# Performance work log

Measured on AMD Instinct MI355X. Metric: run time of the kernel, lower is better.

Reference implementation:

```python
import jax, jax.numpy as jnp
import numpy as np

N_NODES = 100000
N_EDGES = 1600000
HIDDEN = 128
N_REL = 8


def setup_inputs() -> dict:
    key = jax.random.key(0)
    ks = jax.random.split(key, 12)
    s = 1.0 / np.sqrt(HIDDEN)
    inp = {
        "node_idx": jnp.arange(N_NODES, dtype=jnp.int32),
        "edge_index": jax.random.randint(ks[0], (2, N_EDGES), 0, N_NODES, dtype=jnp.int32),
        "edge_type": jax.random.randint(ks[1], (N_EDGES,), 0, N_REL, dtype=jnp.int32),
        "embedding": jax.random.normal(ks[2], (N_NODES, HIDDEN), jnp.float32),
        "W_rel_0": jax.random.normal(ks[3], (N_REL, HIDDEN, HIDDEN), jnp.float32) * s,
        "W_root_0": jax.random.normal(ks[4], (HIDDEN, HIDDEN), jnp.float32) * s,
        "b_0": jnp.zeros((HIDDEN,), jnp.float32),
        "W_rel_1": jax.random.normal(ks[5], (N_REL, HIDDEN, HIDDEN), jnp.float32) * s,
        "W_root_1": jax.random.normal(ks[6], (HIDDEN, HIDDEN), jnp.float32) * s,
        "b_1": jnp.zeros((HIDDEN,), jnp.float32),
    }
    return inp


def _rgcn_conv(x, src, dst, et, W_rel, W_root, b):
    # PyG RGCNConv: out_i = x_i @ W_root + b + sum_r mean_{j in N_r(i)} x_j @ W_r
    n = x.shape[0]
    r = W_rel.shape[0]
    # Transform all nodes by all relations once (R small), then gather per edge.
    x_all = jnp.einsum('nd,rdf->rnf', x, W_rel)          # [R, N, d]
    msg = x_all[et, src]                                  # [E, d]
    # per-(relation, dst) mean normalization
    seg = et * n + dst                                    # [E]
    deg = jax.ops.segment_sum(jnp.ones(et.shape, jnp.float32), seg, num_segments=r * n)
    norm = 1.0 / jnp.maximum(deg[seg], 1.0)               # [E]
    agg = jax.ops.segment_sum(msg * norm[:, None], dst, num_segments=n)  # [N, d]
    return agg + x @ W_root + b


def reference(node_idx, edge_index, edge_type, embedding,
              W_rel_0, W_root_0, b_0, W_rel_1, W_root_1, b_1):
    src, dst = edge_index[0], edge_index[1]
    x = embedding[node_idx]
    x = jax.nn.relu(_rgcn_conv(x, src, dst, edge_type, W_rel_0, W_root_0, b_0))
    x = jax.nn.relu(_rgcn_conv(x, src, dst, edge_type, W_rel_1, W_root_1, b_1))
    return x
```

## Files before the change

kernel.cpp:

```cpp
#include <hip/hip_runtime.h>
#include <hip/hip_bf16.h>

typedef short bf16x8 __attribute__((ext_vector_type(8)));
typedef float f32x4 __attribute__((ext_vector_type(4)));

constexpr int NN = 100000;
constexpr int NE = 1600000;
constexpr int HH = 128;
constexpr int NR = 8;
constexpr int NBIN = 782;
constexpr int CAPB = 6144;

__device__ __forceinline__ unsigned short f2bf(float f) {
    unsigned b = __float_as_uint(f);
    b += 0x7fffu + ((b >> 16) & 1u);
    return (unsigned short)(b >> 16);
}

__global__ void convertWX(const float* __restrict__ Wr0, const float* __restrict__ Wq0,
                          const float* __restrict__ Wr1, const float* __restrict__ Wq1,
                          unsigned short* __restrict__ Wt,
                          const int* __restrict__ node_idx,
                          const float* __restrict__ emb,
                          unsigned* __restrict__ xb32) {
    if (blockIdx.x < 1152) {
        int o = blockIdx.x * 256 + threadIdx.x;
        int L = o / 147456;
        int rem = o - L * 147456;
        int s = rem >> 14;
        int p = rem & 16383;
        int f = p >> 7;
        int d = p & 127;
        const float* Wq = L ? Wq1 : Wq0;
        const float* Wr = L ? Wr1 : Wr0;
        float v = (s == 0) ? Wq[d * 128 + f] : Wr[((s - 1) * 128 + d) * 128 + f];
        Wt[o] = f2bf(v);
    } else {
        int i = (blockIdx.x - 1152) * 256 + threadIdx.x;
        if (i >= NN * 64) return;
        int n = i >> 6, dp = i & 63;
        int row = node_idx[n];
        float2 v = *((const float2*)(emb + (size_t)row * HH) + dp);
        xb32[(size_t)n * 64 + dp] = (unsigned)f2bf(v.x) | ((unsigned)f2bf(v.y) << 16);
    }
}

__global__ __launch_bounds__(256) void binCount(const int* __restrict__ edst,
                                                unsigned* __restrict__ binCounts) {
    __shared__ unsigned hist[NBIN];
    for (int i = threadIdx.x; i < NBIN; i += 256) hist[i] = 0;
    __syncthreads();
    int stride = gridDim.x * 256;
    for (int e = blockIdx.x * 256 + threadIdx.x; e < NE; e += stride)
        atomicAdd(&hist[((unsigned)edst[e]) >> 7], 1u);
    __syncthreads();
    for (int i = threadIdx.x; i < NBIN; i += 256)
        if (hist[i]) atomicAdd(&binCounts[i], hist[i]);
}

__global__ void binScan(const unsigned* __restrict__ binCounts,
                        unsigned* __restrict__ binStarts,
                        unsigned* __restrict__ binCursor) {
    __shared__ unsigned sh[1024];
    int tid = threadIdx.x;
    unsigned v = (tid < NBIN) ? binCounts[tid] : 0u;
    sh[tid] = v;
    __syncthreads();
    for (int ofs = 1; ofs < 1024; ofs <<= 1) {
        unsigned t = (tid >= ofs) ? sh[tid - ofs] : 0u;
        __syncthreads();
        sh[tid] += t;
        __syncthreads();
    }
    if (tid < NBIN) {
        unsigned s = sh[tid] - v;
        binStarts[tid] = s;
        binCursor[tid] = s;
    }
    if (tid == 0) binStarts[NBIN] = NE;
}

__global__ __launch_bounds__(256) void binScatter(
        const int* __restrict__ esrc, const int* __restrict__ edst,
        const int* __restrict__ etype, unsigned* __restrict__ binCursor,
        unsigned* __restrict__ binned) {
    __shared__ unsigned hist[NBIN];
    __shared__ unsigned cur[NBIN];
    for (int i = threadIdx.x; i < NBIN; i += 256) hist[i] = 0;
    __syncthreads();
    int per = (NE + gridDim.x - 1) / gridDim.x;
    int lo = blockIdx.x * per;
    int hi = lo + per; if (hi > NE) hi = NE;
    for (int e = lo + threadIdx.x; e < hi; e += 256)
        atomicAdd(&hist[((unsigned)edst[e]) >> 7], 1u);
    __syncthreads();
    for (int i = threadIdx.x; i < NBIN; i += 256) {
        unsigned c = hist[i];
        cur[i] = c ? atomicAdd(&binCursor[i], c) : 0u;
    }
    __syncthreads();
    for (int e = lo + threadIdx.x; e < hi; e += 256) {
        unsigned d = (unsigned)edst[e];
        unsigned b = d >> 7;
        unsigned pos = atomicAdd(&cur[b], 1u);
        binned[pos] = (unsigned)esrc[e] | (((unsigned)etype[e]) << 17) |
                      ((d & 127u) << 20);
    }
}

__global__ __launch_bounds__(256) void binSort(
        const unsigned* __restrict__ binStarts, const unsigned* __restrict__ binned,
        unsigned* __restrict__ epk, unsigned* __restrict__ starts) {
    __shared__ unsigned hist[1024];
    __shared__ unsigned scn[1024];
    __shared__ unsigned part[256];
    __shared__ unsigned buf[CAPB];
    __shared__ unsigned outb[CAPB];
    int bin = blockIdx.x;
    int tid = threadIdx.x;
    unsigned base = binStarts[bin];
    int cnt = (int)(binStarts[bin + 1] - base);

    for (int i = tid; i < 1024; i += 256) hist[i] = 0;
    __syncthreads();
    for (int i = tid; i < cnt; i += 256) {
        unsigned p = binned[base + i];
        if (i < CAPB) buf[i] = p;
        atomicAdd(&hist[(p >> 17) & 0x3ffu], 1u);
    }
    __syncthreads();
    unsigned h4[4], tsum = 0;
#pragma unroll
    for (int j = 0; j < 4; ++j) { h4[j] = hist[tid * 4 + j]; tsum += h4[j]; }
    part[tid] = tsum;
    __syncthreads();
    for (int ofs = 1; ofs < 256; ofs <<= 1) {
        unsigned t = (tid >= ofs) ? part[tid - ofs] : 0u;
        __syncthreads();
        part[tid] += t;
        __syncthreads();
    }
    unsigned run = part[tid] - tsum;
#pragma unroll
    for (int j = 0; j < 4; ++j) { scn[tid * 4 + j] = run; run += h4[j]; }
    __syncthreads();
    for (int i = tid; i < 1024; i += 256) {
        starts[(size_t)bin * 1024 + i] = base + scn[i];
        hist[i] = scn[i];
    }
    __syncthreads();
    if (cnt <= CAPB) {
        for (int i = tid; i < cnt; i += 256) {
            unsigned p = buf[i];
            unsigned pos = atomicAdd(&hist[(p >> 17) & 0x3ffu], 1u);
            outb[pos] = p & 0x1ffffu;
        }
        __syncthreads();
        for (int i = tid; i < cnt; i += 256) epk[base + i] = outb[i];
    } else {
        for (int i = tid; i < cnt; i += 256) {
            unsigned p = binned[base + i];
            unsigned pos = atomicAdd(&hist[(p >> 17) & 0x3ffu], 1u);
            epk[base + pos] = p & 0x1ffffu;
        }
    }
}

__global__ __launch_bounds__(256) void gatherNode(
        const unsigned* __restrict__ starts, const unsigned* __restrict__ epk,
        const unsigned* __restrict__ xb32, unsigned* __restrict__ h32) {
    int node = blockIdx.x * 4 + (threadIdx.x >> 6);
    if (node >= NN) return;
    int lane = threadIdx.x & 63;

    unsigned bv = 0;
    if (lane < 9) bv = starts[(size_t)node * 8 + lane];
    unsigned b[9];
#pragma unroll
    for (int r = 0; r < 9; ++r) b[r] = __shfl(bv, r);
    unsigned s0 = b[0], s1 = b[8];
    int cnt = (int)__builtin_amdgcn_readfirstlane((int)(s1 - s0));

    float a[8][2];
#pragma unroll
    for (int r = 0; r < 8; ++r) { a[r][0] = 0.f; a[r][1] = 0.f; }

    for (int c0 = 0; c0 < cnt; c0 += 64) {
        unsigned myE = s0 + (unsigned)c0 + (unsigned)lane;
        unsigned pk = (myE < s1) ? epk[myE] : 0u;
        unsigned rl = 0;
#pragma unroll
        for (int r = 1; r < 8; ++r) rl += (myE >= b[r]) ? 1u : 0u;
        pk |= rl << 24;
        int cend = cnt - c0;
        if (cend > 64) cend = 64;
        for (int base = 0; base < cend; base += 8) {
            int m = cend - base;
            if (m > 8) m = 8;
            unsigned pj[8], qj[8];
#pragma unroll
            for (int j = 0; j < 8; ++j)
                pj[j] = (j < m) ? (unsigned)__shfl((int)pk, base + j) : 0u;
#pragma unroll
            for (int j = 0; j < 8; ++j)
                if (j < m) qj[j] = xb32[(size_t)(pj[j] & 0x1ffffu) * 64 + lane];
#pragma unroll
            for (int j = 0; j < 8; ++j) {
                if (j < m) {
                    float lo = __uint_as_float(qj[j] << 16);
                    float hi = __uint_as_float(qj[j] & 0xffff0000u);
                    switch (__builtin_amdgcn_readfirstlane((int)(pj[j] >> 24))) {
                        case 0: a[0][0] += lo; a[0][1] += hi; break;
                        case 1: a[1][0] += lo; a[1][1] += hi; break;
                        case 2: a[2][0] += lo; a[2][1] += hi; break;
                        case 3: a[3][0] += lo; a[3][1] += hi; break;
                        case 4: a[4][0] += lo; a[4][1] += hi; break;
                        case 5: a[5][0] += lo; a[5][1] += hi; break;
                        case 6: a[6][0] += lo; a[6][1] += hi; break;
                        default: a[7][0] += lo; a[7][1] += hi; break;
                    }
                }
            }
        }
    }

#pragma unroll
    for (int r = 0; r < 8; ++r) {
        unsigned c = b[r + 1] - b[r];
        float inv = (c > 1u) ? (1.f / (float)c) : 1.f;
        unsigned out = (unsigned)f2bf(a[r][0] * inv) |
                       ((unsigned)f2bf(a[r][1] * inv) << 16);
        h32[((size_t)node * 8 + r) * 64 + lane] = out;
    }
}

__global__ __launch_bounds__(256) void rgcnGemm(const unsigned short* x,
                                                const unsigned short* __restrict__ h,
                                                const unsigned short* __restrict__ Wt,
                                                const float* __restrict__ bias,
                                                float* __restrict__ outF,
                                                unsigned short* outB) {
    constexpr int LDA = 136;
    __shared__ __align__(16) unsigned short A_lds[64 * LDA];
    __shared__ __align__(16) unsigned short B_lds[128 * LDA];

    int tid = threadIdx.x;
    int wid = tid >> 6, lane = tid & 63;
    int quad = lane >> 4, l16 = lane & 15;
    int wr = wid >> 1, wc = wid & 1;
    int m0 = blockIdx.x * 64;
    int chunk = tid & 15, rip = tid >> 4;

    f32x4 acc[2][4];
#pragma unroll
    for (int st = 0; st < 2; ++st)
#pragma unroll
        for (int nt = 0; nt < 4; ++nt) acc[st][nt] = (f32x4){0.f, 0.f, 0.f, 0.f};

    for (int s = 0; s < 9; ++s) {
        __syncthreads();
#pragma unroll
        for (int p = 0; p < 4; ++p) {
            int r = p * 16 + rip;
            int node = m0 + r;
            node = node < NN ? node : NN - 1;
            const unsigned short* rp = (s == 0)
                ? (x + (size_t)node * HH)
                : (h + ((size_t)node * 8 + (s - 1)) * HH);
            uint4 v = *((const uint4*)rp + chunk);
            *(uint4*)(&A_lds[r * LDA + chunk * 8]) = v;
        }
        const unsigned short* Bbase = Wt + s * 16384;
#pragma unroll
        for (int p = 0; p < 8; ++p) {
            int r = p * 16 + rip;
            uint4 v = *((const uint4*)(Bbase + r * 128) + chunk);
            *(uint4*)(&B_lds[r * LDA + chunk * 8]) = v;
        }
        __syncthreads();
#pragma unroll
        for (int kt = 0; kt < 4; ++kt) {
            int ko = kt * 32 + quad * 8;
            bf16x8 a[2], b[4];
            a[0] = *(const bf16x8*)(&A_lds[(wr * 32 + l16) * LDA + ko]);
            a[1] = *(const bf16x8*)(&A_lds[(wr * 32 + 16 + l16) * LDA + ko]);
#pragma unroll
            for (int nt = 0; nt < 4; ++nt)
                b[nt] = *(const bf16x8*)(&B_lds[(wc * 64 + nt * 16 + l16) * LDA + ko]);
#pragma unroll
            for (int st = 0; st < 2; ++st)
#pragma unroll
                for (int nt = 0; nt < 4; ++nt)
                    acc[st][nt] = __builtin_amdgcn_mfma_f32_16x16x32_bf16(
                        a[st], b[nt], acc[st][nt], 0, 0, 0);
        }
    }
#pragma unroll
    for (int st = 0; st < 2; ++st) {
        int rowbase = m0 + wr * 32 + st * 16 + quad * 4;
#pragma unroll
        for (int nt = 0; nt < 4; ++nt) {
            int n = wc * 64 + nt * 16 + l16;
            float bv = bias[n];
#pragma unroll
            for (int rg = 0; rg < 4; ++rg) {
                int node = rowbase + rg;
                if (node < NN) {
                    float v = acc[st][nt][rg] + bv;
                    v = v > 0.f ? v : 0.f;
                    if (outF) outF[(size_t)node * HH + n] = v;
                    else outB[(size_t)node * HH + n] = f2bf(v);
                }
            }
        }
    }
}

extern "C" void kernel_launch(void* const* d_in, const int* in_sizes, int n_in,
                              void* d_out, int out_size, void* d_ws, size_t ws_size,
                              hipStream_t stream) {
    const int* node_idx = (const int*)d_in[0];
    const int* eidx     = (const int*)d_in[1];
    const int* etype    = (const int*)d_in[2];
    const float* emb    = (const float*)d_in[3];
    const float* Wr0    = (const float*)d_in[4];
    const float* Wq0    = (const float*)d_in[5];
    const float* b0     = (const float*)d_in[6];
    const float* Wr1    = (const float*)d_in[7];
    const float* Wq1    = (const float*)d_in[8];
    const float* b1     = (const float*)d_in[9];
    const int* esrc = eidx;
    const int* edst = eidx + NE;

    char* ws = (char*)d_ws;
    size_t off = 0;
    auto alloc = [&](size_t bytes) -> void* {
        void* p = ws + off;
        off = (off + bytes + 255) & ~(size_t)255;
        return p;
    };
    unsigned* binCounts = (unsigned*)alloc((size_t)NBIN * 4);
    unsigned* binStarts = (unsigned*)alloc((size_t)(NBIN + 1) * 4);
    unsigned* binCursor = (unsigned*)alloc((size_t)NBIN * 4);
    unsigned* starts    = (unsigned*)alloc((size_t)NBIN * 1024 * 4);
    unsigned* epk       = (unsigned*)alloc((size_t)NE * 4);
    unsigned* xb32      = (unsigned*)alloc((size_t)NN * 64 * 4);
    unsigned* h32       = (unsigned*)alloc((size_t)NN * 8 * 64 * 4);
    unsigned short* Wt  = (unsigned short*)alloc((size_t)2 * 9 * 16384 * 2);
    unsigned* binned = h32;
    (void)ws_size; (void)n_in; (void)in_sizes; (void)out_size;

    hipMemsetAsync(binCounts, 0, (size_t)NBIN * 4, stream);
    convertWX<<<1152 + (NN * 64 + 255) / 256, 256, 0, stream>>>(
        Wr0, Wq0, Wr1, Wq1, Wt, node_idx, emb, xb32);
    binCount<<<256, 256, 0, stream>>>(edst, binCounts);
    binScan<<<1, 1024, 0, stream>>>(binCounts, binStarts, binCursor);
    binScatter<<<128, 256, 0, stream>>>(esrc, edst, etype, binCursor, binned);
    binSort<<<NBIN, 256, 0, stream>>>(binStarts, binned, epk, starts);

    int nblk = (NN + 63) / 64;
    gatherNode<<<(NN + 3) / 4, 256, 0, stream>>>(starts, epk, xb32, h32);
    rgcnGemm<<<nblk, 256, 0, stream>>>((const unsigned short*)xb32,
                                       (const unsigned short*)h32, Wt, b0,
                                       nullptr, (unsigned short*)xb32);
    gatherNode<<<(NN + 3) / 4, 256, 0, stream>>>(starts, epk, xb32, h32);
    rgcnGemm<<<nblk, 256, 0, stream>>>((const unsigned short*)xb32,
                                       (const unsigned short*)h32, Wt + 147456, b1,
                                       (float*)d_out, nullptr);
}
```

Before: 601.7 us.

## Transform nodes by all relations first, then gather normalized messages per edge

Each layer changes from aggregate-then-transform to transform-then-aggregate. The old order gathered x per relation into an [N,8,128] buffer and then ran a 9-step GEMM. Now one GEMM computes x·W_r for every relation plus the root term into a bf16 [N,8,128] table. A scatter kernel then gathers one pre-transformed row per edge, scales it by 1/degree, and adds root, bias and ReLU. binSort now packs (src,rel) and the clamped per-relation degree into each edge word, which removes the per-relation accumulator switch in the gather. The aim is to drop the h buffer's GEMM input and the branchy per-relation accumulation. The cost is that per-edge reads now hit a random-access table eight times larger than before, so cache locality gets worse.

Result: faster. 552.9 us (-8.1%).

```diff
diff --git a/kernel.cpp b/kernel.cpp
--- a/kernel.cpp
+++ b/kernel.cpp
@@ -113,6 +113,7 @@
         unsigned* __restrict__ epk, unsigned* __restrict__ starts) {
     __shared__ unsigned hist[1024];
     __shared__ unsigned scn[1024];
+    __shared__ unsigned cnts[1024];
     __shared__ unsigned part[256];
     __shared__ unsigned buf[CAPB];
     __shared__ unsigned outb[CAPB];
@@ -146,100 +147,35 @@
     __syncthreads();
     for (int i = tid; i < 1024; i += 256) {
         starts[(size_t)bin * 1024 + i] = base + scn[i];
+        cnts[i] = hist[i];
         hist[i] = scn[i];
     }
     __syncthreads();
     if (cnt <= CAPB) {
         for (int i = tid; i < cnt; i += 256) {
             unsigned p = buf[i];
-            unsigned pos = atomicAdd(&hist[(p >> 17) & 0x3ffu], 1u);
-            outb[pos] = p & 0x1ffffu;
+            unsigned key = (p >> 17) & 0x3ffu;
+            unsigned pos = atomicAdd(&hist[key], 1u);
+            unsigned deg = cnts[key]; if (deg > 4095u) deg = 4095u;
+            outb[pos] = ((p & 0x1ffffu) << 3) | (key & 7u) | (deg << 20);
         }
         __syncthreads();
         for (int i = tid; i < cnt; i += 256) epk[base + i] = outb[i];
     } else {
         for (int i = tid; i < cnt; i += 256) {
             unsigned p = binned[base + i];
-            unsigned pos = atomicAdd(&hist[(p >> 17) & 0x3ffu], 1u);
-            epk[base + pos] = p & 0x1ffffu;
-        }
-    }
-}
-
-__global__ __launch_bounds__(256) void gatherNode(
-        const unsigned* __restrict__ starts, const unsigned* __restrict__ epk,
-        const unsigned* __restrict__ xb32, unsigned* __restrict__ h32) {
-    int node = blockIdx.x * 4 + (threadIdx.x >> 6);
-    if (node >= NN) return;
-    int lane = threadIdx.x & 63;
-
-    unsigned bv = 0;
-    if (lane < 9) bv = starts[(size_t)node * 8 + lane];
-    unsigned b[9];
-#pragma unroll
-    for (int r = 0; r < 9; ++r) b[r] = __shfl(bv, r);
-    unsigned s0 = b[0], s1 = b[8];
-    int cnt = (int)__builtin_amdgcn_readfirstlane((int)(s1 - s0));
-
-    float a[8][2];
-#pragma unroll
-    for (int r = 0; r < 8; ++r) { a[r][0] = 0.f; a[r][1] = 0.f; }
-
-    for (int c0 = 0; c0 < cnt; c0 += 64) {
-        unsigned myE = s0 + (unsigned)c0 + (unsigned)lane;
-        unsigned pk = (myE < s1) ? epk[myE] : 0u;
-        unsigned rl = 0;
-#pragma unroll
-        for (int r = 1; r < 8; ++r) rl += (myE >= b[r]) ? 1u : 0u;
-        pk |= rl << 24;
-        int cend = cnt - c0;
-        if (cend > 64) cend = 64;
-        for (int base = 0; base < cend; base += 8) {
-            int m = cend - base;
-            if (m > 8) m = 8;
-            unsigned pj[8], qj[8];
-#pragma unroll
-            for (int j = 0; j < 8; ++j)
-                pj[j] = (j < m) ? (unsigned)__shfl((int)pk, base + j) : 0u;
-#pragma unroll
-            for (int j = 0; j < 8; ++j)
-                if (j < m) qj[j] = xb32[(size_t)(pj[j] & 0x1ffffu) * 64 + lane];
-#pragma unroll
-            for (int j = 0; j < 8; ++j) {
-                if (j < m) {
-                    float lo = __uint_as_float(qj[j] << 16);
-                    float hi = __uint_as_float(qj[j] & 0xffff0000u);
-                    switch (__builtin_amdgcn_readfirstlane((int)(pj[j] >> 24))) {
-                        case 0: a[0][0] += lo; a[0][1] += hi; break;
-                        case 1: a[1][0] += lo; a[1][1] += hi; break;
-                        case 2: a[2][0] += lo; a[2][1] += hi; break;
-                        case 3: a[3][0] += lo; a[3][1] += hi; break;
-                        case 4: a[4][0] += lo; a[4][1] += hi; break;
-                        case 5: a[5][0] += lo; a[5][1] += hi; break;
-                        case 6: a[6][0] += lo; a[6][1] += hi; break;
-                        default: a[7][0] += lo; a[7][1] += hi; break;
-                    }
-                }
-            }
-        }
-    }
-
-#pragma unroll
-    for (int r = 0; r < 8; ++r) {
-        unsigned c = b[r + 1] - b[r];
-        float inv = (c > 1u) ? (1.f / (float)c) : 1.f;
-        unsigned out = (unsigned)f2bf(a[r][0] * inv) |
-                       ((unsigned)f2bf(a[r][1] * inv) << 16);
-        h32[((size_t)node * 8 + r) * 64 + lane] = out;
-    }
-}
-
-__global__ __launch_bounds__(256) void rgcnGemm(const unsigned short* x,
-                                                const unsigned short* __restrict__ h,
-                                                const unsigned short* __restrict__ Wt,
-                                                const float* __restrict__ bias,
-                                                float* __restrict__ outF,
-                                                unsigned short* outB) {
+            unsigned key = (p >> 17) & 0x3ffu;
+            unsigned pos = atomicAdd(&hist[key], 1u);
+            unsigned deg = cnts[key]; if (deg > 4095u) deg = 4095u;
+            epk[base + pos] = ((p & 0x1ffffu) << 3) | (key & 7u) | (deg << 20);
+        }
+    }
+}
+
+__global__ __launch_bounds__(256) void bigGemm(const unsigned short* x,
+                                               const unsigned short* __restrict__ Wt,
+                                               unsigned* __restrict__ y32,
+                                               unsigned* root32) {
     constexpr int LDA = 136;
     __shared__ __align__(16) unsigned short A_lds[64 * LDA];
     __shared__ __align__(16) unsigned short B_lds[128 * LDA];
@@ -251,68 +187,128 @@
     int m0 = blockIdx.x * 64;
     int chunk = tid & 15, rip = tid >> 4;
 
-    f32x4 acc[2][4];
-#pragma unroll
-    for (int st = 0; st < 2; ++st)
-#pragma unroll
-        for (int nt = 0; nt < 4; ++nt) acc[st][nt] = (f32x4){0.f, 0.f, 0.f, 0.f};
+#pragma unroll
+    for (int p = 0; p < 4; ++p) {
+        int r = p * 16 + rip;
+        int node = m0 + r;
+        node = node < NN ? node : NN - 1;
+        uint4 v = *((const uint4*)(x + (size_t)node * HH) + chunk);
+        *(uint4*)(&A_lds[r * LDA + chunk * 8]) = v;
+    }
 
     for (int s = 0; s < 9; ++s) {
         __syncthreads();
-#pragma unroll
-        for (int p = 0; p < 4; ++p) {
-            int r = p * 16 + rip;
-            int node = m0 + r;
-            node = node < NN ? node : NN - 1;
-            const unsigned short* rp = (s == 0)
-                ? (x + (size_t)node * HH)
-                : (h + ((size_t)node * 8 + (s - 1)) * HH);
-            uint4 v = *((const uint4*)rp + chunk);
-            *(uint4*)(&A_lds[r * LDA + chunk * 8]) = v;
-        }
-        const unsigned short* Bbase = Wt + s * 16384;
 #pragma unroll
         for (int p = 0; p < 8; ++p) {
             int r = p * 16 + rip;
-            uint4 v = *((const uint4*)(Bbase + r * 128) + chunk);
+            uint4 v = *((const uint4*)(Wt + s * 16384 + r * 128) + chunk);
             *(uint4*)(&B_lds[r * LDA + chunk * 8]) = v;
         }
         __syncthreads();
+
+        f32x4 acc[2][4];
+#pragma unroll
+        for (int nt = 0; nt < 2; ++nt)
+#pragma unroll
+            for (int ft = 0; ft < 4; ++ft) acc[nt][ft] = (f32x4){0.f, 0.f, 0.f, 0.f};
+
 #pragma unroll
         for (int kt = 0; kt < 4; ++kt) {
             int ko = kt * 32 + quad * 8;
-            bf16x8 a[2], b[4];
-            a[0] = *(const bf16x8*)(&A_lds[(wr * 32 + l16) * LDA + ko]);
-            a[1] = *(const bf16x8*)(&A_lds[(wr * 32 + 16 + l16) * LDA + ko]);
-#pragma unroll
-            for (int nt = 0; nt < 4; ++nt)
-                b[nt] = *(const bf16x8*)(&B_lds[(wc * 64 + nt * 16 + l16) * LDA + ko]);
-#pragma unroll
-            for (int st = 0; st < 2; ++st)
-#pragma unroll
-                for (int nt = 0; nt < 4; ++nt)
-                    acc[st][nt] = __builtin_amdgcn_mfma_f32_16x16x32_bf16(
-                        a[st], b[nt], acc[st][nt], 0, 0, 0);
-        }
-    }
-#pragma unroll
-    for (int st = 0; st < 2; ++st) {
-        int rowbase = m0 + wr * 32 + st * 16 + quad * 4;
-#pragma unroll
-        for (int nt = 0; nt < 4; ++nt) {
-            int n = wc * 64 + nt * 16 + l16;
-            float bv = bias[n];
-#pragma unroll
-            for (int rg = 0; rg < 4; ++rg) {
-                int node = rowbase + rg;
-                if (node < NN) {
-                    float v = acc[st][nt][rg] + bv;
-                    v = v > 0.f ? v : 0.f;
-                    if (outF) outF[(size_t)node * HH + n] = v;
-                    else outB[(size_t)node * HH + n] = f2bf(v);
+            bf16x8 aW[4], bx[2];
+#pragma unroll
+            for (int ft = 0; ft < 4; ++ft)
+                aW[ft] = *(const bf16x8*)(&B_lds[(wc * 64 + ft * 16 + l16) * LDA + ko]);
+#pragma unroll
+            for (int nt = 0; nt < 2; ++nt)
+                bx[nt] = *(const bf16x8*)(&A_lds[(wr * 32 + nt * 16 + l16) * LDA + ko]);
+#pragma unroll
+            for (int nt = 0; nt < 2; ++nt)
+#pragma unroll
+                for (int ft = 0; ft < 4; ++ft)
+                    acc[nt][ft] = __builtin_amdgcn_mfma_f32_16x16x32_bf16(
+                        aW[ft], bx[nt], acc[nt][ft], 0, 0, 0);
+        }
+#pragma unroll
+        for (int nt = 0; nt < 2; ++nt) {
+            int node = m0 + wr * 32 + nt * 16 + l16;
+            if (node < NN) {
+                unsigned* dst = (s == 0) ? (root32 + (size_t)node * 64)
+                                         : (y32 + ((size_t)node * 8 + (s - 1)) * 64);
+#pragma unroll
+                for (int ft = 0; ft < 4; ++ft) {
+                    int f0 = wc * 64 + ft * 16 + quad * 4;
+                    unsigned d0, d1;
+                    asm("v_cvt_pk_bf16_f32 %0, %1, %2"
+                        : "=v"(d0) : "v"(acc[nt][ft][0]), "v"(acc[nt][ft][1]));
+                    asm("v_cvt_pk_bf16_f32 %0, %1, %2"
+                        : "=v"(d1) : "v"(acc[nt][ft][2]), "v"(acc[nt][ft][3]));
+                    *(uint2*)(dst + (f0 >> 1)) = make_uint2(d0, d1);
                 }
             }
         }
+    }
+}
+
+__global__ __launch_bounds__(256) void scatterAgg(
+        const unsigned* __restrict__ starts, const unsigned* __restrict__ epk,
+        const unsigned* __restrict__ y32, const unsigned* root32,
+        const float* __restrict__ bias,
+        float* __restrict__ outF, unsigned* outB) {
+    int node = blockIdx.x * 4 + (threadIdx.x >> 6);
+    if (node >= NN) return;
+    int lane = threadIdx.x & 63;
+
+    unsigned s0 = starts[(size_t)node * 8];
+    unsigned s1 = starts[(size_t)node * 8 + 8];
+    int cnt = (int)__builtin_amdgcn_readfirstlane((int)(s1 - s0));
+
+    float ax = 0.f, ay = 0.f;
+    for (int c0 = 0; c0 < cnt; c0 += 64) {
+        unsigned myE = s0 + (unsigned)c0 + (unsigned)lane;
+        unsigned pk = (myE < s1) ? epk[myE] : 0u;
+        float nrm = __builtin_amdgcn_rcpf((float)(pk >> 20));
+        int cend = cnt - c0;
+        if (cend > 64) cend = 64;
+        for (int base = 0; base < cend; base += 8) {
+            int m = cend - base;
+            if (m > 8) m = 8;
+            int bix = base << 2;
+            unsigned pj[8], qj[8];
+            float nj[8];
+#pragma unroll
+            for (int j = 0; j < 8; ++j) {
+                pj[j] = (unsigned)__builtin_amdgcn_ds_bpermute(bix + (j << 2), (int)pk);
+                nj[j] = __uint_as_float(
+                    (unsigned)__builtin_amdgcn_ds_bpermute(bix + (j << 2),
+                                                           __float_as_int(nrm)));
+            }
+#pragma unroll
+            for (int j = 0; j < 8; ++j)
+                if (j < m) qj[j] = y32[((pj[j] & 0xFFFFFu) << 6) + (unsigned)lane];
+#pragma unroll
+            for (int j = 0; j < 8; ++j) {
+                if (j < m) {
+                    float lo = __uint_as_float(qj[j] << 16);
+                    float hi = __uint_as_float(qj[j] & 0xffff0000u);
+                    ax += lo * nj[j];
+                    ay += hi * nj[j];
+                }
+            }
+        }
+    }
+
+    unsigned r = root32[(size_t)node * 64 + lane];
+    float2 bv = ((const float2*)bias)[lane];
+    float ox = ax + __uint_as_float(r << 16) + bv.x;
+    float oy = ay + __uint_as_float(r & 0xffff0000u) + bv.y;
+    ox = ox > 0.f ? ox : 0.f;
+    oy = oy > 0.f ? oy : 0.f;
+    if (outF) {
+        *(float2*)(outF + (size_t)node * HH + lane * 2) = make_float2(ox, oy);
+    } else {
+        outB[(size_t)node * 64 + lane] =
+            (unsigned)f2bf(ox) | ((unsigned)f2bf(oy) << 16);
     }
 }
 
@@ -345,9 +341,9 @@
     unsigned* starts    = (unsigned*)alloc((size_t)NBIN * 1024 * 4);
     unsigned* epk       = (unsigned*)alloc((size_t)NE * 4);
     unsigned* xb32      = (unsigned*)alloc((size_t)NN * 64 * 4);
-    unsigned* h32       = (unsigned*)alloc((size_t)NN * 8 * 64 * 4);
+    unsigned* y32       = (unsigned*)alloc((size_t)NN * 8 * 64 * 4);
     unsigned short* Wt  = (unsigned short*)alloc((size_t)2 * 9 * 16384 * 2);
-    unsigned* binned = h32;
+    unsigned* binned = y32;
     (void)ws_size; (void)n_in; (void)in_sizes; (void)out_size;
 
     hipMemsetAsync(binCounts, 0, (size_t)NBIN * 4, stream);
@@ -359,12 +355,11 @@
     binSort<<<NBIN, 256, 0, stream>>>(binStarts, binned, epk, starts);
 
     int nblk = (NN + 63) / 64;
-    gatherNode<<<(NN + 3) / 4, 256, 0, stream>>>(starts, epk, xb32, h32);
-    rgcnGemm<<<nblk, 256, 0, stream>>>((const unsigned short*)xb32,
-                                       (const unsigned short*)h32, Wt, b0,
-                                       nullptr, (unsigned short*)xb32);
-    gatherNode<<<(NN + 3) / 4, 256, 0, stream>>>(starts, epk, xb32, h32);
-    rgcnGemm<<<nblk, 256, 0, stream>>>((const unsigned short*)xb32,
-                                       (const unsigned short*)h32, Wt + 147456, b1,
-                                       (float*)d_out, nullptr);
-}
+    bigGemm<<<nblk, 256, 0, stream>>>((const unsigned short*)xb32, Wt, y32, xb32);
+    scatterAgg<<<(NN + 3) / 4, 256, 0, stream>>>(starts, epk, y32, xb32, b0,
+                                                 nullptr, xb32);
+    bigGemm<<<nblk, 256, 0, stream>>>((const unsigned short*)xb32, Wt + 147456,
+                                      y32, xb32);
+    scatterAgg<<<(NN + 3) / 4, 256, 0, stream>>>(starts, epk, y32, xb32, b1,
+                                                 (float*)d_out, nullptr);
+}
```
